# Performance work log

Hardware: AMD Instinct MI355X
Metric: run time of the kernel (lower is better)

## Reference

```python
import jax, jax.numpy as jnp
import numpy as np

B, V, E, L = 1024, 50000, 256, 17  # batch, nodeNum(vocab), embeddingSize, Huffman path length


def setup_inputs() -> dict:
    key = jax.random.key(0)
    k1, k2, k3, k4, k5 = jax.random.split(key, 5)
    x = jax.random.normal(k1, (B, V), dtype=jnp.float32)
    W = jax.random.normal(k2, (E, V), dtype=jnp.float32) * 0.02  # nn.Linear(nodeNum, embeddingSize).weight
    b = jax.random.normal(k3, (E,), dtype=jnp.float32) * 0.02    # nn.Linear bias
    path_vectors = jax.random.normal(k4, (B, L, E), dtype=jnp.float32)  # gathered treeNode.vector along each target's path
    path_signs = jax.random.randint(k5, (B, L), 0, 2, dtype=jnp.int32)  # 1 == 'left' (+v), 0 == 'right' (-v)
    return {"x": x, "W": W, "b": b, "path_vectors": path_vectors, "path_signs": path_signs}


def reference(x, W, b, path_vectors, path_signs):
    # x = self.embeddingSpace(x)
    emb = x @ W.T + b  # [B, E]
    # direct == 'left' -> +node.vector, 'right' -> -node.vector
    signs = (2 * path_signs - 1).astype(emb.dtype)  # [B, L] in {-1, +1}
    logits = jnp.einsum('ble,be->bl', path_vectors, emb) * signs  # per-node dot
    # output = prod_over_path sigmoid(dot)
    return jnp.prod(jax.nn.sigmoid(logits), axis=-1)  # [B]
```

## Files before the change

kernel.cpp:

```cpp
#include <hip/hip_runtime.h>
#include <hip/hip_bf16.h>
#include <math.h>

#define VDIM 50000
#define BDIM 1024
#define EDIM 256
#define LDIM 17

constexpr int BM = 128, BN = 128, BK = 32;
constexpr int KT_FULL = VDIM / BK;
constexpr int SPLITS  = 64;
constexpr int TAILZ   = KT_FULL % SPLITS;

typedef short bf16x8 __attribute__((ext_vector_type(8)));
typedef float f32x4  __attribute__((ext_vector_type(4)));

__device__ __forceinline__ void async_f4(const float* g, float* l) {
    __builtin_amdgcn_global_load_lds(
        (const __attribute__((address_space(1))) void*)g,
        (__attribute__((address_space(3))) void*)l, 16, 0, 0);
}

__device__ __forceinline__ void split8(const float4 f0, const float4 f1, bf16x8& h, bf16x8& l) {
    const float f[8] = {f0.x, f0.y, f0.z, f0.w, f1.x, f1.y, f1.z, f1.w};
#pragma unroll
    for (int i = 0; i < 8; ++i) {
        const uint32_t u  = __float_as_uint(f[i]);
        h[i] = (short)(u >> 16);
        const float lo = f[i] - __uint_as_float(u & 0xFFFF0000u);
        l[i] = (short)(__float_as_uint(lo) >> 16);
    }
}

__global__ __launch_bounds__(256) void gemm_split3(
    const float* __restrict__ X, const float* __restrict__ Wm, float* __restrict__ emb) {
    __shared__ __align__(16) float sA[BM * BK];
    __shared__ __align__(16) float sB[BN * BK];

    const int tid = threadIdx.x;
    const int bn0 = blockIdx.x * BN;
    const int bm0 = blockIdx.y * BM;
    const int z   = blockIdx.z;

    const int lane = tid & 63;
    const int wv   = tid >> 6;
    const int wm0  = (wv >> 1) * 64;
    const int wn0  = (wv & 1) * 64;
    const int lm   = lane & 15;
    const int gk0  = (lane >> 4) * 2;

    const int rsub   = lane >> 3;
    const int grp    = lane & 7;
    const int coloff = ((grp ^ rsub) << 2);
    const int rowS   = wv * 32 + rsub;

    f32x4 acc[4][4] = {};

    auto compute = [&]() {
        bf16x8 ah[4], al[4];
#pragma unroll
        for (int mi = 0; mi < 4; ++mi) {
            const int row = wm0 + mi * 16 + lm;
            const int s = row & 7;
            const float4 f0 = *reinterpret_cast<const float4*>(&sA[row * BK + ((gk0 ^ s) << 2)]);
            const float4 f1 = *reinterpret_cast<const float4*>(&sA[row * BK + (((gk0 + 1) ^ s) << 2)]);
            split8(f0, f1, ah[mi], al[mi]);
        }
#pragma unroll
        for (int ni = 0; ni < 4; ++ni) {
            const int row = wn0 + ni * 16 + lm;
            const int s = row & 7;
            const float4 f0 = *reinterpret_cast<const float4*>(&sB[row * BK + ((gk0 ^ s) << 2)]);
            const float4 f1 = *reinterpret_cast<const float4*>(&sB[row * BK + (((gk0 + 1) ^ s) << 2)]);
            bf16x8 bh, bl;
            split8(f0, f1, bh, bl);
#pragma unroll
            for (int mi = 0; mi < 4; ++mi) {
                acc[mi][ni] = __builtin_amdgcn_mfma_f32_16x16x32_bf16(ah[mi], bh, acc[mi][ni], 0, 0, 0);
                acc[mi][ni] = __builtin_amdgcn_mfma_f32_16x16x32_bf16(ah[mi], bl, acc[mi][ni], 0, 0, 0);
                acc[mi][ni] = __builtin_amdgcn_mfma_f32_16x16x32_bf16(al[mi], bh, acc[mi][ni], 0, 0, 0);
            }
        }
    };

    for (int kt = z; kt < KT_FULL; kt += SPLITS) {
        const int k0 = kt * BK;
        __syncthreads();
#pragma unroll
        for (int j = 0; j < 4; ++j) {
            const int row = rowS + j * 8;
            async_f4(X  + (size_t)(bm0 + row) * VDIM + k0 + coloff, &sA[(wv * 32 + j * 8) * BK]);
            async_f4(Wm + (size_t)(bn0 + row) * VDIM + k0 + coloff, &sB[(wv * 32 + j * 8) * BK]);
        }
        __syncthreads();
        compute();
    }

    if (z == TAILZ) {
        const int k0 = KT_FULL * BK;
        __syncthreads();
#pragma unroll
        for (int j = 0; j < 4; ++j) {
            const int row = rowS + j * 8;
            float4 va = make_float4(0.f, 0.f, 0.f, 0.f), vb = va;
            if (coloff < 16) {
                va = *reinterpret_cast<const float4*>(X  + (size_t)(bm0 + row) * VDIM + k0 + coloff);
                vb = *reinterpret_cast<const float4*>(Wm + (size_t)(bn0 + row) * VDIM + k0 + coloff);
            }
            *reinterpret_cast<float4*>(&sA[row * BK + (grp << 2)]) = va;
            *reinterpret_cast<float4*>(&sB[row * BK + (grp << 2)]) = vb;
        }
        __syncthreads();
        compute();
    }

    const int orow = (lane >> 4) * 4;
#pragma unroll
    for (int mi = 0; mi < 4; ++mi)
#pragma unroll
        for (int ni = 0; ni < 4; ++ni)
#pragma unroll
            for (int r = 0; r < 4; ++r) {
                const int gm = bm0 + wm0 + mi * 16 + orow + r;
                const int gn = bn0 + wn0 + ni * 16 + lm;
                atomicAdd(&emb[gm * EDIM + gn], acc[mi][ni][r]);
            }
}

__global__ __launch_bounds__(256) void stage2_kernel(
    const float* __restrict__ emb, const float* __restrict__ bias,
    const float* __restrict__ pv, const int* __restrict__ signs,
    float* __restrict__ out) {
    const int b = blockIdx.x;
    __shared__ float se[EDIM];
    __shared__ float wp[4];
    const int t = threadIdx.x;
    se[t] = emb[b * EDIM + t] + bias[t];
    __syncthreads();
    const int w = t >> 6, lane = t & 63;
    float p = 1.0f;
    for (int l = w; l < LDIM; l += 4) {
        const float4 a = *reinterpret_cast<const float4*>(&pv[((size_t)b * LDIM + l) * EDIM + lane * 4]);
        const float4 e = *reinterpret_cast<const float4*>(&se[lane * 4]);
        float d = a.x * e.x + a.y * e.y + a.z * e.z + a.w * e.w;
#pragma unroll
        for (int off = 32; off > 0; off >>= 1) d += __shfl_xor(d, off, 64);
        const float zz = signs[b * LDIM + l] ? d : -d;
        p *= 1.0f / (1.0f + expf(-zz));
    }
    if (lane == 0) wp[w] = p;
    __syncthreads();
    if (t == 0) out[b] = wp[0] * wp[1] * wp[2] * wp[3];
}

extern "C" void kernel_launch(void* const* d_in, const int* in_sizes, int n_in,
                              void* d_out, int out_size, void* d_ws, size_t ws_size,
                              hipStream_t stream) {
    const float* X    = (const float*)d_in[0];
    const float* Wm   = (const float*)d_in[1];
    const float* bias = (const float*)d_in[2];
    const float* pv   = (const float*)d_in[3];
    const int*   sg   = (const int*)d_in[4];
    float* out = (float*)d_out;
    float* emb = (float*)d_ws;

    hipMemsetAsync(emb, 0, (size_t)BDIM * EDIM * sizeof(float), stream);

    dim3 grid(EDIM / BN, BDIM / BM, SPLITS);
    gemm_split3<<<grid, 256, 0, stream>>>(X, Wm, emb);

    stage2_kernel<<<BDIM, 256, 0, stream>>>(emb, bias, pv, sg, out);
}
```

Baseline: 423.0 us.

## Double-buffer split-K GEMM tiles and halve the K-split count

The GEMM kernel now keeps two LDS buffers per operand. It issues the async global-to-LDS loads for the next K tile before computing on the current one, so memory latency can overlap with the bf16 split MFMA work. The number of K splits drops from 64 to 32, which gives longer per-block loops to pipeline and fewer atomic adds into the output. In exchange, LDS use per block doubles, which can lower occupancy, and the grid has fewer blocks. The overlap also depends on the compiler not inserting a full vmcnt wait before the LDS reads.

```diff
diff --git a/kernel.cpp b/kernel.cpp
--- a/kernel.cpp
+++ b/kernel.cpp
@@ -9,7 +9,7 @@
 
 constexpr int BM = 128, BN = 128, BK = 32;
 constexpr int KT_FULL = VDIM / BK;
-constexpr int SPLITS  = 64;
+constexpr int SPLITS  = 32;
 constexpr int TAILZ   = KT_FULL % SPLITS;
 
 typedef short bf16x8 __attribute__((ext_vector_type(8)));
@@ -34,8 +34,8 @@
 
 __global__ __launch_bounds__(256) void gemm_split3(
     const float* __restrict__ X, const float* __restrict__ Wm, float* __restrict__ emb) {
-    __shared__ __align__(16) float sA[BM * BK];
-    __shared__ __align__(16) float sB[BN * BK];
+    __shared__ __align__(16) float sA[2][BM * BK];
+    __shared__ __align__(16) float sB[2][BN * BK];
 
     const int tid = threadIdx.x;
     const int bn0 = blockIdx.x * BN;
@@ -56,22 +56,34 @@
 
     f32x4 acc[4][4] = {};
 
-    auto compute = [&]() {
+    auto issue = [&](int kt, int pb) {
+        const int k0 = kt * BK;
+#pragma unroll
+        for (int j = 0; j < 4; ++j) {
+            const int row = rowS + j * 8;
+            async_f4(X  + (size_t)(bm0 + row) * VDIM + k0 + coloff, &sA[pb][(wv * 32 + j * 8) * BK]);
+            async_f4(Wm + (size_t)(bn0 + row) * VDIM + k0 + coloff, &sB[pb][(wv * 32 + j * 8) * BK]);
+        }
+    };
+
+    auto compute = [&](int pb) {
+        const float* A = sA[pb];
+        const float* Bs = sB[pb];
         bf16x8 ah[4], al[4];
 #pragma unroll
         for (int mi = 0; mi < 4; ++mi) {
             const int row = wm0 + mi * 16 + lm;
             const int s = row & 7;
-            const float4 f0 = *reinterpret_cast<const float4*>(&sA[row * BK + ((gk0 ^ s) << 2)]);
-            const float4 f1 = *reinterpret_cast<const float4*>(&sA[row * BK + (((gk0 + 1) ^ s) << 2)]);
+            const float4 f0 = *reinterpret_cast<const float4*>(&A[row * BK + ((gk0 ^ s) << 2)]);
+            const float4 f1 = *reinterpret_cast<const float4*>(&A[row * BK + (((gk0 + 1) ^ s) << 2)]);
             split8(f0, f1, ah[mi], al[mi]);
         }
 #pragma unroll
         for (int ni = 0; ni < 4; ++ni) {
             const int row = wn0 + ni * 16 + lm;
             const int s = row & 7;
-            const float4 f0 = *reinterpret_cast<const float4*>(&sB[row * BK + ((gk0 ^ s) << 2)]);
-            const float4 f1 = *reinterpret_cast<const float4*>(&sB[row * BK + (((gk0 + 1) ^ s) << 2)]);
+            const float4 f0 = *reinterpret_cast<const float4*>(&Bs[row * BK + ((gk0 ^ s) << 2)]);
+            const float4 f1 = *reinterpret_cast<const float4*>(&Bs[row * BK + (((gk0 + 1) ^ s) << 2)]);
             bf16x8 bh, bl;
             split8(f0, f1, bh, bl);
 #pragma unroll
@@ -83,22 +95,19 @@
         }
     };
 
-    for (int kt = z; kt < KT_FULL; kt += SPLITS) {
-        const int k0 = kt * BK;
+    int pb = 0;
+    issue(z, 0);
+    for (int kt = z + SPLITS; kt < KT_FULL; kt += SPLITS) {
         __syncthreads();
-#pragma unroll
-        for (int j = 0; j < 4; ++j) {
-            const int row = rowS + j * 8;
-            async_f4(X  + (size_t)(bm0 + row) * VDIM + k0 + coloff, &sA[(wv * 32 + j * 8) * BK]);
-            async_f4(Wm + (size_t)(bn0 + row) * VDIM + k0 + coloff, &sB[(wv * 32 + j * 8) * BK]);
-        }
-        __syncthreads();
-        compute();
+        issue(kt, pb ^ 1);
+        compute(pb);
+        pb ^= 1;
     }
+    __syncthreads();
+    compute(pb);
 
     if (z == TAILZ) {
         const int k0 = KT_FULL * BK;
-        __syncthreads();
 #pragma unroll
         for (int j = 0; j < 4; ++j) {
             const int row = rowS + j * 8;
@@ -107,11 +116,11 @@
                 va = *reinterpret_cast<const float4*>(X  + (size_t)(bm0 + row) * VDIM + k0 + coloff);
                 vb = *reinterpret_cast<const float4*>(Wm + (size_t)(bn0 + row) * VDIM + k0 + coloff);
             }
-            *reinterpret_cast<float4*>(&sA[row * BK + (grp << 2)]) = va;
-            *reinterpret_cast<float4*>(&sB[row * BK + (grp << 2)]) = vb;
+            *reinterpret_cast<float4*>(&sA[pb ^ 1][row * BK + (grp << 2)]) = va;
+            *reinterpret_cast<float4*>(&sB[pb ^ 1][row * BK + (grp << 2)]) = vb;
         }
         __syncthreads();
-        compute();
+        compute(pb ^ 1);
     }
 
     const int orow = (lane >> 4) * 4;
```

Measured after the change: 398.7 us. -5.8%, faster.

## Load GEMM operands directly from global into registers, drop LDS staging

Applied to the files above, without the earlier changes.

Removes the shared-memory tiles and async global-to-LDS copies. Each lane now loads its MFMA fragments straight from global memory into registers, which removes both __syncthreads per K tile and the LDS reads. The grid is also reordered so split-K index varies fastest, changing which blocks run together and how they share cache. The cost is that waves with overlapping rows fetch the same data again from cache instead of LDS. The per-lane accesses are 32-byte chunks spread across many rows, so they coalesce less well than before.

```diff
diff --git a/kernel.cpp b/kernel.cpp
--- a/kernel.cpp
+++ b/kernel.cpp
@@ -15,12 +15,6 @@
 typedef short bf16x8 __attribute__((ext_vector_type(8)));
 typedef float f32x4  __attribute__((ext_vector_type(4)));
 
-__device__ __forceinline__ void async_f4(const float* g, float* l) {
-    __builtin_amdgcn_global_load_lds(
-        (const __attribute__((address_space(1))) void*)g,
-        (__attribute__((address_space(3))) void*)l, 16, 0, 0);
-}
-
 __device__ __forceinline__ void split8(const float4 f0, const float4 f1, bf16x8& h, bf16x8& l) {
     const float f[8] = {f0.x, f0.y, f0.z, f0.w, f1.x, f1.y, f1.z, f1.w};
 #pragma unroll
@@ -34,84 +28,79 @@
 
 __global__ __launch_bounds__(256) void gemm_split3(
     const float* __restrict__ X, const float* __restrict__ Wm, float* __restrict__ emb) {
-    __shared__ __align__(16) float sA[BM * BK];
-    __shared__ __align__(16) float sB[BN * BK];
-
     const int tid = threadIdx.x;
-    const int bn0 = blockIdx.x * BN;
+    const int z   = blockIdx.x;
     const int bm0 = blockIdx.y * BM;
-    const int z   = blockIdx.z;
+    const int bn0 = blockIdx.z * BN;
 
     const int lane = tid & 63;
     const int wv   = tid >> 6;
     const int wm0  = (wv >> 1) * 64;
     const int wn0  = (wv & 1) * 64;
     const int lm   = lane & 15;
-    const int gk0  = (lane >> 4) * 2;
+    const int kg   = lane >> 4;
 
-    const int rsub   = lane >> 3;
-    const int grp    = lane & 7;
-    const int coloff = ((grp ^ rsub) << 2);
-    const int rowS   = wv * 32 + rsub;
+    size_t rowA[4], rowB[4];
+#pragma unroll
+    for (int i = 0; i < 4; ++i) {
+        rowA[i] = (size_t)(bm0 + wm0 + i * 16 + lm) * VDIM;
+        rowB[i] = (size_t)(bn0 + wn0 + i * 16 + lm) * VDIM;
+    }
 
     f32x4 acc[4][4] = {};
 
-    auto compute = [&]() {
-        bf16x8 ah[4], al[4];
+    auto do_tile = [&](const float4 a[4][2], const float4 b[4][2]) {
+        bf16x8 ah[4], al[4], bh[4], bl[4];
 #pragma unroll
-        for (int mi = 0; mi < 4; ++mi) {
-            const int row = wm0 + mi * 16 + lm;
-            const int s = row & 7;
-            const float4 f0 = *reinterpret_cast<const float4*>(&sA[row * BK + ((gk0 ^ s) << 2)]);
-            const float4 f1 = *reinterpret_cast<const float4*>(&sA[row * BK + (((gk0 + 1) ^ s) << 2)]);
-            split8(f0, f1, ah[mi], al[mi]);
-        }
+        for (int i = 0; i < 4; ++i) split8(a[i][0], a[i][1], ah[i], al[i]);
 #pragma unroll
-        for (int ni = 0; ni < 4; ++ni) {
-            const int row = wn0 + ni * 16 + lm;
-            const int s = row & 7;
-            const float4 f0 = *reinterpret_cast<const float4*>(&sB[row * BK + ((gk0 ^ s) << 2)]);
-            const float4 f1 = *reinterpret_cast<const float4*>(&sB[row * BK + (((gk0 + 1) ^ s) << 2)]);
-            bf16x8 bh, bl;
-            split8(f0, f1, bh, bl);
+        for (int i = 0; i < 4; ++i) split8(b[i][0], b[i][1], bh[i], bl[i]);
 #pragma unroll
-            for (int mi = 0; mi < 4; ++mi) {
-                acc[mi][ni] = __builtin_amdgcn_mfma_f32_16x16x32_bf16(ah[mi], bh, acc[mi][ni], 0, 0, 0);
-                acc[mi][ni] = __builtin_amdgcn_mfma_f32_16x16x32_bf16(ah[mi], bl, acc[mi][ni], 0, 0, 0);
-                acc[mi][ni] = __builtin_amdgcn_mfma_f32_16x16x32_bf16(al[mi], bh, acc[mi][ni], 0, 0, 0);
+        for (int mi = 0; mi < 4; ++mi)
+#pragma unroll
+            for (int ni = 0; ni < 4; ++ni) {
+                acc[mi][ni] = __builtin_amdgcn_mfma_f32_16x16x32_bf16(ah[mi], bh[ni], acc[mi][ni], 0, 0, 0);
+                acc[mi][ni] = __builtin_amdgcn_mfma_f32_16x16x32_bf16(ah[mi], bl[ni], acc[mi][ni], 0, 0, 0);
+                acc[mi][ni] = __builtin_amdgcn_mfma_f32_16x16x32_bf16(al[mi], bh[ni], acc[mi][ni], 0, 0, 0);
             }
-        }
     };
 
     for (int kt = z; kt < KT_FULL; kt += SPLITS) {
-        const int k0 = kt * BK;
-        __syncthreads();
+        const size_t k0 = (size_t)kt * BK + kg * 8;
+        float4 a[4][2], b[4][2];
 #pragma unroll
-        for (int j = 0; j < 4; ++j) {
-            const int row = rowS + j * 8;
-            async_f4(X  + (size_t)(bm0 + row) * VDIM + k0 + coloff, &sA[(wv * 32 + j * 8) * BK]);
-            async_f4(Wm + (size_t)(bn0 + row) * VDIM + k0 + coloff, &sB[(wv * 32 + j * 8) * BK]);
+        for (int i = 0; i < 4; ++i) {
+            const float* pa = X + rowA[i] + k0;
+            a[i][0] = *reinterpret_cast<const float4*>(pa);
+            a[i][1] = *reinterpret_cast<const float4*>(pa + 4);
         }
-        __syncthreads();
-        compute();
+#pragma unroll
+        for (int i = 0; i < 4; ++i) {
+            const float* pb = Wm + rowB[i] + k0;
+            b[i][0] = *reinterpret_cast<const float4*>(pb);
+            b[i][1] = *reinterpret_cast<const float4*>(pb + 4);
+        }
+        do_tile(a, b);
     }
 
     if (z == TAILZ) {
-        const int k0 = KT_FULL * BK;
-        __syncthreads();
+        const size_t k0 = (size_t)KT_FULL * BK + kg * 8;
+        const float4 zf = make_float4(0.f, 0.f, 0.f, 0.f);
+        float4 a[4][2], b[4][2];
 #pragma unroll
-        for (int j = 0; j < 4; ++j) {
-            const int row = rowS + j * 8;
-            float4 va = make_float4(0.f, 0.f, 0.f, 0.f), vb = va;
-            if (coloff < 16) {
-                va = *reinterpret_cast<const float4*>(X  + (size_t)(bm0 + row) * VDIM + k0 + coloff);
-                vb = *reinterpret_cast<const float4*>(Wm + (size_t)(bn0 + row) * VDIM + k0 + coloff);
+        for (int i = 0; i < 4; ++i) {
+            a[i][0] = a[i][1] = zf;
+            b[i][0] = b[i][1] = zf;
+            if (kg < 2) {
+                const float* pa = X + rowA[i] + k0;
+                const float* pb = Wm + rowB[i] + k0;
+                a[i][0] = *reinterpret_cast<const float4*>(pa);
+                a[i][1] = *reinterpret_cast<const float4*>(pa + 4);
+                b[i][0] = *reinterpret_cast<const float4*>(pb);
+                b[i][1] = *reinterpret_cast<const float4*>(pb + 4);
             }
-            *reinterpret_cast<float4*>(&sA[row * BK + (grp << 2)]) = va;
-            *reinterpret_cast<float4*>(&sB[row * BK + (grp << 2)]) = vb;
         }
-        __syncthreads();
-        compute();
+        do_tile(a, b);
     }
 
     const int orow = (lane >> 4) * 4;
@@ -166,7 +155,7 @@
 
     hipMemsetAsync(emb, 0, (size_t)BDIM * EDIM * sizeof(float), stream);
 
-    dim3 grid(EDIM / BN, BDIM / BM, SPLITS);
+    dim3 grid(SPLITS, BDIM / BM, EDIM / BN);
     gemm_split3<<<grid, 256, 0, stream>>>(X, Wm, emb);
 
     stage2_kernel<<<BDIM, 256, 0, stream>>>(emb, bias, pv, sg, out);
```

New measurement: 468.8 us. +10.8%, slower.
